# Optimization experiments

Measured on AMD Instinct MI355X. Metric: run time of the kernel, lower is better.

The kernel has to match this reference:

```python
import jax, jax.numpy as jnp
import numpy as np

EPS = 1e-6


def _forward(x, weight_compress, weight_expand, body_w1, body_b1, body_w2, body_b2,
             route_w, route_b, off_w, off_b, out_h, out_w):
    b, C, h, w = x.shape
    E, r, _ = weight_compress.shape
    scale_h = out_h / h
    scale_w = out_w / w

    # --- scale-aware coordinate features: [out_h, out_w, 4] ---
    ch = (jnp.arange(out_h, dtype=jnp.float32) + 0.5) / scale_h
    coor_h = ch - jnp.floor(ch + EPS) - 0.5            # [H]
    cw = (jnp.arange(out_w, dtype=jnp.float32) + 0.5) / scale_w
    coor_w = cw - jnp.floor(cw + EPS) - 0.5            # [W]
    ones = jnp.ones((out_h, out_w), jnp.float32)
    feat = jnp.stack([ones / scale_w, ones / scale_h,
                      coor_h[:, None] * ones, coor_w[None, :] * ones], axis=-1)

    # --- body (1x1 convs == per-pixel MLP), routing, offset ---
    emb = jax.nn.gelu(feat @ body_w1.T + body_b1, approximate=False)
    emb = jax.nn.gelu(emb @ body_w2.T + body_b2, approximate=False)   # [H,W,64]
    routing = jax.nn.sigmoid(emb @ route_w.T + route_b)               # [H,W,E]
    offset = emb @ off_w.T + off_b                                    # [H,W,2]

    # --- per-pixel soft-MoE weight mixing ---
    rw = routing.reshape(-1, E)                                       # [HW,E]
    wc = (rw @ weight_compress.reshape(E, -1)).reshape(out_h, out_w, r, C)
    we = (rw @ weight_expand.reshape(E, -1)).reshape(out_h, out_w, C, r)

    # --- grid_sample with learned offsets (bilinear, zero padding, align_corners=False) ---
    gx = ((jnp.arange(out_w, dtype=jnp.float32) + 0.5) / scale_w - 0.5) * 2.0 / (w - 1) - 1.0
    gy = ((jnp.arange(out_h, dtype=jnp.float32) + 0.5) / scale_h - 0.5) * 2.0 / (h - 1) - 1.0
    gx2 = gx[None, :] + offset[..., 0] * 2.0 / (w - 1)                # [H,W]
    gy2 = gy[:, None] + offset[..., 1] * 2.0 / (h - 1)                # [H,W]
    ix = (gx2 + 1.0) * w / 2.0 - 0.5
    iy = (gy2 + 1.0) * h / 2.0 - 0.5
    x0 = jnp.floor(ix); x1 = x0 + 1.0
    y0 = jnp.floor(iy); y1 = y0 + 1.0
    wx1 = ix - x0; wx0 = 1.0 - wx1
    wy1 = iy - y0; wy0 = 1.0 - wy1

    def gather(yy, xx):
        valid = ((xx >= 0) & (xx <= w - 1) & (yy >= 0) & (yy <= h - 1)).astype(x.dtype)
        xi = jnp.clip(xx, 0, w - 1).astype(jnp.int32)
        yi = jnp.clip(yy, 0, h - 1).astype(jnp.int32)
        return x[:, :, yi, xi] * valid[None, None]                    # [B,C,H,W]

    fea0 = (gather(y0, x0) * (wy0 * wx0)[None, None]
            + gather(y0, x1) * (wy0 * wx1)[None, None]
            + gather(y1, x0) * (wy1 * wx0)[None, None]
            + gather(y1, x1) * (wy1 * wx1)[None, None])               # [B,C,H,W]

    # --- per-pixel dynamic compress/expand matmuls ---
    mid = jnp.einsum('hwrc,bchw->bhwr', wc, fea0)
    out = jnp.einsum('hwcr,bhwr->bchw', we, mid)
    return out + fea0


def setup_inputs() -> dict:
    key = jax.random.key(0)
    ks = jax.random.split(key, 12)
    C, E, r, hid = 64, 4, 4, 64
    s = 0.1
    return {
        'x': jax.random.normal(ks[0], (4, C, 192, 192), jnp.float32),
        'weight_compress': jax.random.normal(ks[1], (E, r, C), jnp.float32) * s,
        'weight_expand': jax.random.normal(ks[2], (E, C, r), jnp.float32) * s,
        'body_w1': jax.random.normal(ks[3], (hid, 4), jnp.float32) * 0.5,
        'body_b1': jax.random.normal(ks[4], (hid,), jnp.float32) * 0.1,
        'body_w2': jax.random.normal(ks[5], (hid, hid), jnp.float32) * (1.0 / np.sqrt(hid)),
        'body_b2': jax.random.normal(ks[6], (hid,), jnp.float32) * 0.1,
        'route_w': jax.random.normal(ks[7], (E, hid), jnp.float32) * (1.0 / np.sqrt(hid)),
        'route_b': jax.random.normal(ks[8], (E,), jnp.float32) * 0.1,
        'off_w': jax.random.normal(ks[9], (2, hid), jnp.float32) * (1.0 / np.sqrt(hid)),
        'off_b': jax.random.normal(ks[10], (2,), jnp.float32) * 0.1,
        'out_h': 384,
        'out_w': 384,
    }


def reference(x, weight_compress, weight_expand, body_w1, body_b1, body_w2, body_b2,
              route_w, route_b, off_w, off_b, out_h, out_w):
    return _forward(x, weight_compress, weight_expand, body_w1, body_b1, body_w2,
                    body_b2, route_w, route_b, off_w, off_b, out_h, out_w)
```

## Files before the change

kernel.cpp:

```cpp
#include <hip/hip_runtime.h>
#include <math.h>

#define BB 4
#define CC 64
#define IH 192
#define IW 192
#define OH 384
#define OW 384
#define NE 4
#define NR 4
#define HID 64

__device__ __forceinline__ float gelu_exact(float v) {
    return 0.5f * v * (1.0f + erff(v * 0.70710678118654752f));
}

__global__ void precompute_kernel(
    const float* __restrict__ wcomp, const float* __restrict__ wexp,
    const float* __restrict__ bw1, const float* __restrict__ bb1,
    const float* __restrict__ bw2, const float* __restrict__ bb2,
    const float* __restrict__ rw, const float* __restrict__ rb,
    const float* __restrict__ ow, const float* __restrict__ ob,
    float* __restrict__ ws)
{
    __shared__ float s_e1[4][HID];
    __shared__ float s_e2[4][HID];
    __shared__ float s_rt[4][NE];
    const int tid = threadIdx.x;
    const int p = tid >> 6;
    const int j = tid & 63;
    const float ch = (p & 2) ? 0.25f : -0.25f;
    const float cw = (p & 1) ? 0.25f : -0.25f;
    float a = bw1[j*4+0]*0.5f + bw1[j*4+1]*0.5f + bw1[j*4+2]*ch + bw1[j*4+3]*cw + bb1[j];
    s_e1[p][j] = gelu_exact(a);
    __syncthreads();
    float acc = bb2[j];
    #pragma unroll 8
    for (int k = 0; k < HID; ++k) acc += bw2[j*HID+k]*s_e1[p][k];
    s_e2[p][j] = gelu_exact(acc);
    __syncthreads();
    if (j < NE) {
        float s = rb[j];
        for (int k = 0; k < HID; ++k) s += rw[j*HID+k]*s_e2[p][k];
        s_rt[p][j] = 1.0f/(1.0f+expf(-s));
    } else if (j < NE+2) {
        const int d = j - NE;
        float s = ob[d];
        for (int k = 0; k < HID; ++k) s += ow[d*HID+k]*s_e2[p][k];
        ws[2048 + p*2 + d] = s;
    }
    __syncthreads();
    const int c = j;
    const float r0 = s_rt[p][0], r1 = s_rt[p][1], r2 = s_rt[p][2], r3 = s_rt[p][3];
    #pragma unroll
    for (int r = 0; r < NR; ++r) {
        float v = r0*wcomp[0*NR*CC + r*CC + c] + r1*wcomp[1*NR*CC + r*CC + c]
                + r2*wcomp[2*NR*CC + r*CC + c] + r3*wcomp[3*NR*CC + r*CC + c];
        ws[(p*CC + c)*4 + r] = v;
        float u = r0*wexp[0*CC*NR + c*NR + r] + r1*wexp[1*CC*NR + c*NR + r]
                + r2*wexp[2*CC*NR + c*NR + r] + r3*wexp[3*CC*NR + c*NR + r];
        ws[1024 + (p*CC + c)*4 + r] = u;
    }
}

__global__ __launch_bounds__(256, 4) void upsample_kernel(
    const float* __restrict__ x, const float* __restrict__ ws,
    float* __restrict__ out)
{
    __shared__ __align__(16) float s_tab[2056];
    for (int i = threadIdx.x; i < 2056; i += 256) s_tab[i] = ws[i];
    __syncthreads();

    const int idx = blockIdx.x * 256 + threadIdx.x;
    const int b   = idx / (OH*OW);
    const int rem = idx - b*(OH*OW);
    const int oy  = rem / OW;
    const int ox  = rem - oy*OW;
    const int p   = ((oy & 1) << 1) | (ox & 1);

    const float offx = s_tab[2048 + p*2 + 0];
    const float offy = s_tab[2048 + p*2 + 1];

    const float inv_w1 = 2.0f / 191.0f;
    float gx2 = (((ox + 0.5f)*0.5f - 0.5f) * inv_w1 - 1.0f) + offx * inv_w1;
    float gy2 = (((oy + 0.5f)*0.5f - 0.5f) * inv_w1 - 1.0f) + offy * inv_w1;
    float ix = (gx2 + 1.0f) * 96.0f - 0.5f;
    float iy = (gy2 + 1.0f) * 96.0f - 0.5f;

    float x0f = floorf(ix), y0f = floorf(iy);
    float wx1 = ix - x0f, wx0 = 1.0f - wx1;
    float wy1 = iy - y0f, wy0 = 1.0f - wy1;
    float x1f = x0f + 1.0f, y1f = y0f + 1.0f;
    float vx0 = (x0f >= 0.0f && x0f <= 191.0f) ? 1.0f : 0.0f;
    float vx1 = (x1f >= 0.0f && x1f <= 191.0f) ? 1.0f : 0.0f;
    float vy0 = (y0f >= 0.0f && y0f <= 191.0f) ? 1.0f : 0.0f;
    float vy1 = (y1f >= 0.0f && y1f <= 191.0f) ? 1.0f : 0.0f;
    const float w00 = wy0*wx0*vy0*vx0;
    const float w01 = wy0*wx1*vy0*vx1;
    const float w10 = wy1*wx0*vy1*vx0;
    const float w11 = wy1*wx1*vy1*vx1;

    const int xi0 = (int)fminf(fmaxf(x0f, 0.0f), 191.0f);
    const int xi1 = (int)fminf(fmaxf(x1f, 0.0f), 191.0f);
    const int yi0 = (int)fminf(fmaxf(y0f, 0.0f), 191.0f);
    const int yi1 = (int)fminf(fmaxf(y1f, 0.0f), 191.0f);

    const float* __restrict__ xb = x + (size_t)b * (CC*IH*IW);
    const int o00 = yi0*IW + xi0;
    const int o01 = yi0*IW + xi1;
    const int o10 = yi1*IW + xi0;
    const int o11 = yi1*IW + xi1;

    const float4* wc4 = ((const float4*)s_tab) + p*CC;
    const float4* we4 = ((const float4*)s_tab) + 256 + p*CC;

    float f[CC];
    float mid0 = 0.f, mid1 = 0.f, mid2 = 0.f, mid3 = 0.f;
    #pragma unroll
    for (int c = 0; c < CC; ++c) {
        const int o = c*IH*IW;
        float v = w00*xb[o+o00] + w01*xb[o+o01] + w10*xb[o+o10] + w11*xb[o+o11];
        f[c] = v;
        float4 wc = wc4[c];
        mid0 += wc.x*v; mid1 += wc.y*v; mid2 += wc.z*v; mid3 += wc.w*v;
    }
    float* __restrict__ op = out + (size_t)b * (CC*OH*OW) + oy*OW + ox;
    #pragma unroll
    for (int c = 0; c < CC; ++c) {
        float4 we = we4[c];
        op[c*OH*OW] = f[c] + we.x*mid0 + we.y*mid1 + we.z*mid2 + we.w*mid3;
    }
}

extern "C" void kernel_launch(void* const* d_in, const int* in_sizes, int n_in,
                              void* d_out, int out_size, void* d_ws, size_t ws_size,
                              hipStream_t stream) {
    const float* x     = (const float*)d_in[0];
    const float* wcomp = (const float*)d_in[1];
    const float* wexp  = (const float*)d_in[2];
    const float* bw1   = (const float*)d_in[3];
    const float* bb1   = (const float*)d_in[4];
    const float* bw2   = (const float*)d_in[5];
    const float* bb2   = (const float*)d_in[6];
    const float* rw    = (const float*)d_in[7];
    const float* rb    = (const float*)d_in[8];
    const float* ow    = (const float*)d_in[9];
    const float* ob    = (const float*)d_in[10];
    float* ws  = (float*)d_ws;
    float* out = (float*)d_out;

    precompute_kernel<<<1, 256, 0, stream>>>(wcomp, wexp, bw1, bb1, bw2, bb2,
                                             rw, rb, ow, ob, ws);
    const int total = BB*OH*OW;
    upsample_kernel<<<total/256, 256, 0, stream>>>(x, ws, out);
}
```

Measured before the change: 240.5 us.

## Split channels across four wavefronts per pixel with shared-memory mid reduction

Each block now covers 64 pixels, and four wavefronts each handle 16 of the 64 channels instead of one thread doing all channels. The partial compress sums are reduced through shared memory after a barrier, and the expanded outputs are written with nontemporal stores. This cuts per-thread register pressure (f[64] down to f[16]) and gives four times more threads to hide gather latency. The cost is an extra barrier, shared-memory traffic, and redundant coordinate math in each wavefront.

```diff
diff --git a/kernel.cpp b/kernel.cpp
--- a/kernel.cpp
+++ b/kernel.cpp
@@ -68,12 +68,16 @@
     float* __restrict__ out)
 {
     __shared__ __align__(16) float s_tab[2056];
-    for (int i = threadIdx.x; i < 2056; i += 256) s_tab[i] = ws[i];
+    __shared__ float4 s_mid[4][64];
+    const int lane = threadIdx.x;
+    const int cg   = threadIdx.y;
+    const int tid  = cg*64 + lane;
+    for (int i = tid; i < 2056; i += 256) s_tab[i] = ws[i];
     __syncthreads();
 
-    const int idx = blockIdx.x * 256 + threadIdx.x;
-    const int b   = idx / (OH*OW);
-    const int rem = idx - b*(OH*OW);
+    const int pix = blockIdx.x * 64 + lane;
+    const int b   = pix / (OH*OW);
+    const int rem = pix - b*(OH*OW);
     const int oy  = rem / OW;
     const int ox  = rem - oy*OW;
     const int p   = ((oy & 1) << 1) | (ox & 1);
@@ -105,30 +109,40 @@
     const int yi0 = (int)fminf(fmaxf(y0f, 0.0f), 191.0f);
     const int yi1 = (int)fminf(fmaxf(y1f, 0.0f), 191.0f);
 
-    const float* __restrict__ xb = x + (size_t)b * (CC*IH*IW);
     const int o00 = yi0*IW + xi0;
     const int o01 = yi0*IW + xi1;
     const int o10 = yi1*IW + xi0;
     const int o11 = yi1*IW + xi1;
 
-    const float4* wc4 = ((const float4*)s_tab) + p*CC;
-    const float4* we4 = ((const float4*)s_tab) + 256 + p*CC;
+    const float* __restrict__ xb = x + b*(CC*IH*IW) + cg*(16*IH*IW);
+    const float4* wc4 = ((const float4*)s_tab) + p*CC + cg*16;
+    const float4* we4 = ((const float4*)s_tab) + 256 + p*CC + cg*16;
 
-    float f[CC];
-    float mid0 = 0.f, mid1 = 0.f, mid2 = 0.f, mid3 = 0.f;
+    float f[16];
+    float4 mid = make_float4(0.f, 0.f, 0.f, 0.f);
     #pragma unroll
-    for (int c = 0; c < CC; ++c) {
-        const int o = c*IH*IW;
+    for (int j = 0; j < 16; ++j) {
+        const int o = j*(IH*IW);
         float v = w00*xb[o+o00] + w01*xb[o+o01] + w10*xb[o+o10] + w11*xb[o+o11];
-        f[c] = v;
-        float4 wc = wc4[c];
-        mid0 += wc.x*v; mid1 += wc.y*v; mid2 += wc.z*v; mid3 += wc.w*v;
+        f[j] = v;
+        float4 wc = wc4[j];
+        mid.x += wc.x*v; mid.y += wc.y*v; mid.z += wc.z*v; mid.w += wc.w*v;
     }
-    float* __restrict__ op = out + (size_t)b * (CC*OH*OW) + oy*OW + ox;
+    s_mid[cg][lane] = mid;
+    __syncthreads();
+    float4 m0 = s_mid[0][lane], m1 = s_mid[1][lane],
+           m2 = s_mid[2][lane], m3 = s_mid[3][lane];
+    const float mid0 = m0.x + m1.x + m2.x + m3.x;
+    const float mid1 = m0.y + m1.y + m2.y + m3.y;
+    const float mid2 = m0.z + m1.z + m2.z + m3.z;
+    const float mid3 = m0.w + m1.w + m2.w + m3.w;
+
+    float* __restrict__ op = out + b*(CC*OH*OW) + cg*(16*OH*OW) + oy*OW + ox;
     #pragma unroll
-    for (int c = 0; c < CC; ++c) {
-        float4 we = we4[c];
-        op[c*OH*OW] = f[c] + we.x*mid0 + we.y*mid1 + we.z*mid2 + we.w*mid3;
+    for (int j = 0; j < 16; ++j) {
+        float4 we = we4[j];
+        float v = f[j] + we.x*mid0 + we.y*mid1 + we.z*mid2 + we.w*mid3;
+        __builtin_nontemporal_store(v, op + j*(OH*OW));
     }
 }
 
@@ -151,6 +165,7 @@
 
     precompute_kernel<<<1, 256, 0, stream>>>(wcomp, wexp, bw1, bb1, bw2, bb2,
                                              rw, rb, ow, ob, ws);
-    const int total = BB*OH*OW;
-    upsample_kernel<<<total/256, 256, 0, stream>>>(x, ws, out);
+    const int total_pix = BB*OH*OW;
+    dim3 block(64, 4);
+    upsample_kernel<<<total_pix/64, block, 0, stream>>>(x, ws, out);
 }
```

After: 243.5 us. Within noise of the previous version (+1.3%).
